# Performance work log

Measured on AMD Instinct MI355X. Metric: run time of the kernel, lower is better.

Reference implementation:

```python
import jax, jax.numpy as jnp
import numpy as np

B, S, DIM = 2, 2048, 2048
H = 16
Q_LORA, KV_LORA = 512, 512
D_NOPE, D_ROPE, D_V = 128, 64, 128
D_QK = D_NOPE + D_ROPE  # 192
SCALE = D_QK ** -0.5
EPS = 1e-6


def rmsnorm(x, w):
    return x * jax.lax.rsqrt(jnp.mean(x * x, axis=-1, keepdims=True) + EPS) * w


def apply_rope(x, cos, sin):
    # x: [B, S, h, d] with d even; cos/sin: [S, d//2] (complex-pair rotation)
    xs = x.reshape(*x.shape[:-1], -1, 2)
    x0, x1 = xs[..., 0], xs[..., 1]
    c = cos[None, :, None, :]
    s = sin[None, :, None, :]
    out = jnp.stack([x0 * c - x1 * s, x0 * s + x1 * c], axis=-1)
    return out.reshape(x.shape)


def setup_inputs() -> dict:
    key = jax.random.key(0)
    ks = jax.random.split(key, 8)
    std = 0.02
    x = jax.random.normal(ks[0], (B, S, DIM), dtype=jnp.float32)
    wq_a_w = jax.random.normal(ks[1], (DIM, Q_LORA), dtype=jnp.float32) * std
    wq_a_b = jnp.zeros((Q_LORA,), dtype=jnp.float32)
    q_norm_w = jnp.ones((Q_LORA,), dtype=jnp.float32)
    wq_b_w = jax.random.normal(ks[2], (Q_LORA, H * D_QK), dtype=jnp.float32) * std
    wkv_a_w = jax.random.normal(ks[3], (DIM, KV_LORA + D_ROPE), dtype=jnp.float32) * std
    wkv_a_b = jnp.zeros((KV_LORA + D_ROPE,), dtype=jnp.float32)
    kv_norm_w = jnp.ones((KV_LORA,), dtype=jnp.float32)
    wkv_b_w = jax.random.normal(ks[4], (KV_LORA, H * (D_NOPE + D_V)), dtype=jnp.float32) * std
    wo_w = jax.random.normal(ks[5], (H * D_V, DIM), dtype=jnp.float32) * std
    # rotary table: freqs_cis[t, i] = exp(1j * t * 10000^{-2i/d})
    inv_freq = 1.0 / (10000.0 ** (np.arange(0, D_ROPE, 2, dtype=np.float32) / D_ROPE))
    t = np.arange(S, dtype=np.float32)
    ang = np.outer(t, inv_freq)  # [S, D_ROPE//2]
    freqs_cos = jnp.asarray(np.cos(ang), dtype=jnp.float32)
    freqs_sin = jnp.asarray(np.sin(ang), dtype=jnp.float32)
    # causal mask (prefill): 0 on/below diagonal, -1e9 above
    mask = jnp.where(jnp.arange(S)[:, None] >= jnp.arange(S)[None, :], 0.0, -1e9).astype(jnp.float32)
    return {"x": x, "wq_a_w": wq_a_w, "wq_a_b": wq_a_b, "q_norm_w": q_norm_w,
            "wq_b_w": wq_b_w, "wkv_a_w": wkv_a_w, "wkv_a_b": wkv_a_b,
            "kv_norm_w": kv_norm_w, "wkv_b_w": wkv_b_w, "wo_w": wo_w,
            "freqs_cos": freqs_cos, "freqs_sin": freqs_sin, "mask": mask,
            "start_pos": 0}


def reference(x, wq_a_w, wq_a_b, q_norm_w, wq_b_w, wkv_a_w, wkv_a_b,
              kv_norm_w, wkv_b_w, wo_w, freqs_cos, freqs_sin, mask, start_pos):
    bsz, seqlen, _ = x.shape
    # low-rank Q: wq_b(q_norm(wq_a(x)))
    q = rmsnorm(x @ wq_a_w + wq_a_b, q_norm_w) @ wq_b_w
    q = q.reshape(bsz, seqlen, H, D_QK)
    q_nope, q_pe = q[..., :D_NOPE], q[..., D_NOPE:]
    q_pe = apply_rope(q_pe, freqs_cos, freqs_sin)
    # low-rank KV
    kv_full = x @ wkv_a_w + wkv_a_b
    kv, k_pe = kv_full[..., :KV_LORA], kv_full[..., KV_LORA:]
    k_pe = apply_rope(k_pe[:, :, None, :], freqs_cos, freqs_sin)  # [B,S,1,D_ROPE]
    kv = rmsnorm(kv, kv_norm_w) @ wkv_b_w
    kv = kv.reshape(bsz, seqlen, H, D_NOPE + D_V)
    k_nope, v = kv[..., :D_NOPE], kv[..., D_NOPE:]
    k = jnp.concatenate([k_nope, jnp.broadcast_to(k_pe, (bsz, seqlen, H, D_ROPE))], axis=-1)
    # prefill (start_pos=0): cache[:, :end_pos] == freshly written k, v
    q = jnp.concatenate([q_nope, q_pe], axis=-1)
    scores = jnp.einsum('bshd,bthd->bsht', q, k) * SCALE
    scores = scores + mask[None, :, None, :]
    attn = jax.nn.softmax(scores.astype(jnp.float32), axis=-1).astype(q.dtype)
    out = jnp.einsum('bsht,bthd->bshd', attn, v)
    return out.reshape(bsz, seqlen, H * D_V) @ wo_w
```

## Files before the change

kernel.cpp:

```cpp
#include <hip/hip_runtime.h>
#include <hip/hip_bf16.h>

typedef unsigned short u16;
typedef unsigned int u32;
typedef __attribute__((ext_vector_type(8))) __bf16 bf16x8;
typedef __attribute__((ext_vector_type(4))) float f32x4;
typedef __attribute__((ext_vector_type(4))) u32 u32x4;
typedef __attribute__((ext_vector_type(2))) u32 u32x2;

#define S_LEN 2048
#define BF16_ONE 0x3F80u

__device__ __forceinline__ float b2f(u16 u) {
  union { unsigned u; float f; } v; v.u = ((unsigned)u) << 16; return v.f;
}
__device__ __forceinline__ u16 f2b(float f) {
  union { float f; unsigned u; } v; v.f = f;
  unsigned r = v.u + 0x7fffu + ((v.u >> 16) & 1u);
  return (u16)(r >> 16);
}
__device__ __forceinline__ u32 cvt_pk_bf16(float a, float b) {
  u32 r;
  asm("v_cvt_pk_bf16_f32 %0, %1, %2" : "=v"(r) : "v"(a), "v"(b));
  return r;
}

__device__ __forceinline__ void glds16(const u16* g, u16* l) {
  __builtin_amdgcn_global_load_lds((const __attribute__((address_space(1))) void*)g,
                                   (__attribute__((address_space(3))) void*)l, 16, 0, 0);
}

__device__ __forceinline__ bool probe_f32(const u16* p) { return p[0] != (u16)BF16_ONE; }

struct CvtDesc {
  const void* src[7];
  u16* dst[7];
  int cum[8];
};
__global__ __launch_bounds__(256) void cvt_batch(CvtDesc d, const u16* __restrict__ probe,
                                                 int total) {
  int i = blockIdx.x * 256 + threadIdx.x;
  if (i >= total) return;
  int t = 0;
#pragma unroll
  for (int k = 1; k < 7; ++k) t += (i >= d.cum[k]);
  int li = i - d.cum[t];
  if (probe_f32(probe)) {
    const float* s = (const float*)d.src[t] + (long)li * 8;
    u16 tmp[8];
#pragma unroll
    for (int j = 0; j < 8; ++j) tmp[j] = f2b(s[j]);
    *(u32x4*)(d.dst[t] + (long)li * 8) = *(const u32x4*)tmp;
  } else {
    *(u32x4*)(d.dst[t] + (long)li * 8) = ((const u32x4*)d.src[t])[li];
  }
}

struct TrDesc {
  const void* in[5];
  u16* out[5];
  int R[5], C[5];
  int tcum[6];
  float scale[5];
};
__global__ __launch_bounds__(256) void transpose_batch(TrDesc d,
                                                       const u16* __restrict__ probe) {
  __shared__ u16 tile[32][33];
  int bid = blockIdx.x;
  int t = 0;
#pragma unroll
  for (int k = 1; k < 5; ++k) t += (bid >= d.tcum[k]);
  int rem = bid - d.tcum[t];
  const int R = d.R[t], C = d.C[t];
  const int tilesX = C >> 5;
  const int bx = rem % tilesX, by = rem / tilesX;
  const int c0 = bx * 32, r0 = by * 32;
  const int tx = threadIdx.x, ty = threadIdx.y;
  const float sc = d.scale[t];
  if (probe_f32(probe)) {
    const float* inf = (const float*)d.in[t];
#pragma unroll
    for (int i = 0; i < 4; ++i)
      tile[ty + i * 8][tx] = f2b(inf[(long)(r0 + ty + i * 8) * C + c0 + tx] * sc);
  } else {
    const u16* inb = (const u16*)d.in[t];
#pragma unroll
    for (int i = 0; i < 4; ++i)
      tile[ty + i * 8][tx] = f2b(b2f(inb[(long)(r0 + ty + i * 8) * C + c0 + tx]) * sc);
  }
  __syncthreads();
  u16* outp = d.out[t];
#pragma unroll
  for (int i = 0; i < 4; ++i)
    outp[(long)(c0 + ty + i * 8) * R + r0 + tx] = tile[tx][ty + i * 8];
}

__global__ __launch_bounds__(256) void transpose_v(const u16* __restrict__ kvb,
                                                   u16* __restrict__ vt) {
  __shared__ u16 tile[32][33];
  int s0 = blockIdx.x * 32, d0 = blockIdx.y * 32, bh = blockIdx.z;
  int b = bh >> 4, h = bh & 15;
  int tx = threadIdx.x, ty = threadIdx.y;
#pragma unroll
  for (int i = 0; i < 4; ++i)
    tile[ty + i * 8][tx] =
        kvb[((long)b * S_LEN + s0 + ty + i * 8) * 4096 + h * 256 + 128 + d0 + tx];
  __syncthreads();
#pragma unroll
  for (int i = 0; i < 4; ++i)
    vt[((long)bh * 128 + d0 + ty + i * 8) * S_LEN + s0 + tx] = tile[tx][ty + i * 8];
}

template <int MT>
__global__ __launch_bounds__(256) void gemm_bt(const u16* __restrict__ A,
                                               const u16* __restrict__ Bt,
                                               const u16* __restrict__ bias,
                                               void* __restrict__ Cv,
                                               int M, int N, int K,
                                               const u16* __restrict__ oprobe) {
  constexpr int MI = MT / 32;
  __shared__ u16 As[2][MT * 32];
  __shared__ u16 Bs[2][128 * 32];
  const int tid = threadIdx.x;
  const int lane = tid & 63;
  const int w = tid >> 6;
  const int quad = lane >> 4;
  const int l16 = lane & 15;
  const int m0 = blockIdx.y * MT;
  const int n0 = blockIdx.x * 128;
  const int wm = (w >> 1) * (MT / 2);
  const int wn = (w & 1) * 64;

  const f32x4 zero = {0.f, 0.f, 0.f, 0.f};
  f32x4 acc[MI][4];
#pragma unroll
  for (int i = 0; i < MI; ++i)
#pragma unroll
    for (int j = 0; j < 4; ++j) acc[i][j] = zero;

  auto stage = [&](int k0, int buf) {
#pragma unroll
    for (int cc = 0; cc < MT * 4; cc += 256) {
      int j = cc + tid, ar = j >> 2, ak = ((j & 3) ^ (ar & 3)) * 8;
      glds16(A + (long)(m0 + ar) * K + k0 + ak, As[buf] + j * 8);
    }
#pragma unroll
    for (int cc = 0; cc < 512; cc += 256) {
      int j = cc + tid, br = j >> 2, bk = ((j & 3) ^ (br & 3)) * 8;
      int bn = n0 + br; if (bn > N - 1) bn = N - 1;
      glds16(Bt + (long)bn * K + k0 + bk, Bs[buf] + j * 8);
    }
  };

  const int nk = K >> 5;
  stage(0, 0);
  for (int t = 0; t < nk; ++t) {
    __syncthreads();
    if (t + 1 < nk) stage((t + 1) << 5, (t + 1) & 1);
    const u16* as = As[t & 1];
    const u16* bs = Bs[t & 1];
    bf16x8 af[MI], bfr[4];
#pragma unroll
    for (int mi = 0; mi < MI; ++mi)
      af[mi] = *(const bf16x8*)(as + (wm + mi * 16 + l16) * 32 +
                                ((quad ^ (l16 & 3)) * 8));
#pragma unroll
    for (int ni = 0; ni < 4; ++ni)
      bfr[ni] = *(const bf16x8*)(bs + (wn + ni * 16 + l16) * 32 +
                                 ((quad ^ (l16 & 3)) * 8));
#pragma unroll
    for (int mi = 0; mi < MI; ++mi)
#pragma unroll
      for (int ni = 0; ni < 4; ++ni)
        acc[mi][ni] = __builtin_amdgcn_mfma_f32_16x16x32_bf16(af[mi], bfr[ni],
                                                              acc[mi][ni], 0, 0, 0);
  }

  u16* C = (u16*)Cv;
  float* Cf = (float*)Cv;
  const bool of32 = oprobe && probe_f32(oprobe);
#pragma unroll
  for (int ni = 0; ni < 4; ++ni) {
    int col = n0 + wn + ni * 16 + l16;
    if (col >= N) continue;
    float bv = bias ? b2f(bias[col]) : 0.0f;
#pragma unroll
    for (int mi = 0; mi < MI; ++mi) {
      int row = m0 + wm + mi * 16 + quad * 4;
#pragma unroll
      for (int r = 0; r < 4; ++r) {
        float val = acc[mi][ni][r] + bv;
        if (of32) Cf[(long)(row + r) * N + col] = val;
        else      C[(long)(row + r) * N + col] = f2b(val);
      }
    }
  }
}

__global__ __launch_bounds__(256) void rmsnorm512(const u16* __restrict__ in, int in_stride,
                                                  const u16* __restrict__ w,
                                                  u16* __restrict__ out, int out_stride) {
  __shared__ float red[4];
  int row = blockIdx.x, tid = threadIdx.x;
  const u16* x = in + (long)row * in_stride;
  float v0 = b2f(x[tid]), v1 = b2f(x[tid + 256]);
  float ss = v0 * v0 + v1 * v1;
#pragma unroll
  for (int off = 1; off < 64; off <<= 1) ss += __shfl_xor(ss, off);
  if ((tid & 63) == 0) red[tid >> 6] = ss;
  __syncthreads();
  float tot = red[0] + red[1] + red[2] + red[3];
  float r = rsqrtf(tot * (1.0f / 512.0f) + 1e-6f);
  u16* y = out + (long)row * out_stride;
  y[tid] = f2b(v0 * r * b2f(w[tid]));
  y[tid + 256] = f2b(v1 * r * b2f(w[tid + 256]));
}

__global__ __launch_bounds__(256) void rope_q_kernel(u16* __restrict__ q,
                                                     const u16* __restrict__ fc,
                                                     const u16* __restrict__ fs) {
  int i = blockIdx.x * 256 + threadIdx.x;
  int pair = i & 31;
  int h = (i >> 5) & 15;
  int row = i >> 9;
  int pos = row & (S_LEN - 1);
  long base = (long)row * 3072 + h * 192 + 128 + pair * 2;
  float x0 = b2f(q[base]), x1 = b2f(q[base + 1]);
  float c = b2f(fc[pos * 32 + pair]), s = b2f(fs[pos * 32 + pair]);
  q[base] = f2b(x0 * c - x1 * s);
  q[base + 1] = f2b(x0 * s + x1 * c);
}

__global__ __launch_bounds__(256) void rope_k_kernel(const u16* __restrict__ kva,
                                                     u16* __restrict__ kpe,
                                                     const u16* __restrict__ fc,
                                                     const u16* __restrict__ fs) {
  int i = blockIdx.x * 256 + threadIdx.x;
  int pair = i & 31;
  int row = i >> 5;
  int pos = row & (S_LEN - 1);
  long sb = (long)row * 576 + 512 + pair * 2;
  float x0 = b2f(kva[sb]), x1 = b2f(kva[sb + 1]);
  float c = b2f(fc[pos * 32 + pair]), s = b2f(fs[pos * 32 + pair]);
  kpe[(long)row * 64 + pair * 2] = f2b(x0 * c - x1 * s);
  kpe[(long)row * 64 + pair * 2 + 1] = f2b(x0 * s + x1 * c);
}

__global__ __launch_bounds__(512, 1) void mla_attn(const u16* __restrict__ q,
                                                   const u16* __restrict__ kvb,
                                                   const u16* __restrict__ vt,
                                                   const u16* __restrict__ kpe,
                                                   u16* __restrict__ o) {
  __shared__ u16 Ks[2][2][64 * 192];
  __shared__ u16 Vts[2][128 * 64];
  const int tid = threadIdx.x;
  const int w = tid >> 6;
  const int g = w >> 2;
  const int sw = w & 3;
  const int lane = tid & 63;
  const int quad = lane >> 4;
  const int l16 = lane & 15;
  const int bh = blockIdx.x;
  const int b = bh >> 4, h = bh & 15;
  const long rowbase = (long)b * S_LEN;
  const f32x4 zero = {0.f, 0.f, 0.f, 0.f};

  auto stage_k = [&](int t0s, u16* dst) {
#pragma unroll
    for (int tt = 0; tt < 3; ++tt) {
      int j = tt * 512 + tid;
      int r = j / 24, csw = j % 24;
      int c = csw ^ (r & 7);
      const u16* src = (c < 16)
                           ? (kvb + (rowbase + t0s + r) * 4096 + h * 256 + c * 8)
                           : (kpe + (rowbase + t0s + r) * 64 + (c - 16) * 8);
      glds16(src, dst + j * 8);
    }
  };
  auto stage_v = [&](int t0s, u16* dst) {
#pragma unroll
    for (int tt = 0; tt < 2; ++tt) {
      int j = tt * 512 + tid;
      int d = j >> 3, c = (j & 7) ^ (d & 7);
      glds16(vt + ((long)bh * 128 + d) * S_LEN + t0s + c * 8, dst + j * 8);
    }
  };

  const int srcA = (((quad & 1) << 1) | (quad >> 1)) * 16 + l16;
  const int srcB = srcA ^ 16;
  const bool lowq = quad < 2;
  const int p = quad & 1;

  const int yy = blockIdx.y;
  const int jt = (yy < 8) ? yy : 23 - yy;
  const int q0 = jt * 128;
  const int ns = jt + 1;
  const int rowlo = q0 + sw * 32;

  const u16* qrowA = q + (rowbase + rowlo + l16) * 3072 + h * 192;
  const u16* qrowB = qrowA + 16 * 3072;
  bf16x8 qfA[6], qfB[6];
#pragma unroll
  for (int kk = 0; kk < 6; ++kk) {
    qfA[kk] = *(const bf16x8*)(qrowA + kk * 32 + quad * 8);
    qfB[kk] = *(const bf16x8*)(qrowB + kk * 32 + quad * 8);
  }

  float mA = -INFINITY, mB = -INFINITY;
  float lA = 0.f, lB = 0.f;
  f32x4 oA[8], oB[8];
#pragma unroll
  for (int i = 0; i < 8; ++i) { oA[i] = zero; oB[i] = zero; }

  auto finish_half = [&](f32x4* s, float& m_r, float& l_r, f32x4* oacc,
                         int lim, bool needmask, bf16x8& ap0, bf16x8& ap1) {
    if (needmask) {
#pragma unroll
      for (int gg = 0; gg < 4; ++gg)
#pragma unroll
        for (int r = 0; r < 4; ++r)
          s[gg][r] = (gg * 16 + r > lim) ? -1e30f : s[gg][r];
    }
    float mx0 = fmaxf(fmaxf(s[0][0], s[0][1]), fmaxf(s[0][2], s[0][3]));
    float mx1 = fmaxf(fmaxf(s[1][0], s[1][1]), fmaxf(s[1][2], s[1][3]));
    float mx2 = fmaxf(fmaxf(s[2][0], s[2][1]), fmaxf(s[2][2], s[2][3]));
    float mx3 = fmaxf(fmaxf(s[3][0], s[3][1]), fmaxf(s[3][2], s[3][3]));
    float vmax = fmaxf(fmaxf(mx0, mx1), fmaxf(mx2, mx3));
    vmax = fmaxf(vmax, __shfl_xor(vmax, 16));
    vmax = fmaxf(vmax, __shfl_xor(vmax, 32));

    if (!__all(vmax <= m_r + 8.0f)) {
      float mnew = fmaxf(m_r, vmax);
      float alpha = __expf(m_r - mnew);
      m_r = mnew;
      l_r *= alpha;
      float al0 = __shfl(alpha, (lane & 48) | (quad * 4 + 0));
      float al1 = __shfl(alpha, (lane & 48) | (quad * 4 + 1));
      float al2 = __shfl(alpha, (lane & 48) | (quad * 4 + 2));
      float al3 = __shfl(alpha, (lane & 48) | (quad * 4 + 3));
#pragma unroll
      for (int nt = 0; nt < 8; ++nt) {
        f32x4 tt = oacc[nt];
        tt[0] *= al0; tt[1] *= al1; tt[2] *= al2; tt[3] *= al3;
        oacc[nt] = tt;
      }
    }

    float e00 = __expf(s[0][0] - m_r), e01 = __expf(s[0][1] - m_r);
    float e02 = __expf(s[0][2] - m_r), e03 = __expf(s[0][3] - m_r);
    float e10 = __expf(s[1][0] - m_r), e11 = __expf(s[1][1] - m_r);
    float e12 = __expf(s[1][2] - m_r), e13 = __expf(s[1][3] - m_r);
    float e20 = __expf(s[2][0] - m_r), e21 = __expf(s[2][1] - m_r);
    float e22 = __expf(s[2][2] - m_r), e23 = __expf(s[2][3] - m_r);
    float e30 = __expf(s[3][0] - m_r), e31 = __expf(s[3][1] - m_r);
    float e32 = __expf(s[3][2] - m_r), e33 = __expf(s[3][3] - m_r);
    l_r += ((e00 + e01) + (e02 + e03)) + ((e10 + e11) + (e12 + e13)) +
           ((e20 + e21) + (e22 + e23)) + ((e30 + e31) + (e32 + e33));
    u32 pk0x = cvt_pk_bf16(e00, e01), pk0y = cvt_pk_bf16(e02, e03);
    u32 pk1x = cvt_pk_bf16(e10, e11), pk1y = cvt_pk_bf16(e12, e13);
    u32 pk2x = cvt_pk_bf16(e20, e21), pk2y = cvt_pk_bf16(e22, e23);
    u32 pk3x = cvt_pk_bf16(e30, e31), pk3y = cvt_pk_bf16(e32, e33);

    u32 a0c = p ? pk1x : pk0x, a1c = p ? pk1y : pk0y;
    u32 a2c = p ? pk3x : pk2x, a3c = p ? pk3y : pk2y;
    u32 b0c = p ? pk0x : pk1x, b1c = p ? pk0y : pk1y;
    u32 b2c = p ? pk2x : pk3x, b3c = p ? pk2y : pk3y;
    u32 A0 = __shfl(a0c, srcA), A1 = __shfl(a1c, srcA);
    u32 A2 = __shfl(a2c, srcA), A3 = __shfl(a3c, srcA);
    u32 B0 = __shfl(b0c, srcB), B1 = __shfl(b1c, srcB);
    u32 B2 = __shfl(b2c, srcB), B3 = __shfl(b3c, srcB);
    u32x4 w0 = {lowq ? A0 : B0, lowq ? A1 : B1, lowq ? B0 : A0, lowq ? B1 : A1};
    u32x4 w1 = {lowq ? A2 : B2, lowq ? A3 : B3, lowq ? B2 : A2, lowq ? B3 : A3};
    ap0 = __builtin_bit_cast(bf16x8, w0);
    ap1 = __builtin_bit_cast(bf16x8, w1);
  };

  stage_k(0, Ks[0][0]);
  stage_k(64, Ks[0][1]);

  for (int i = 0; i < ns; ++i) {
    __syncthreads();
    stage_v((2 * i) * 64, Vts[0]);
    stage_v((2 * i + 1) * 64, Vts[1]);
    if (i + 1 < ns) {
      stage_k((2 * i + 2) * 64, Ks[(i + 1) & 1][0]);
      stage_k((2 * i + 3) * 64, Ks[(i + 1) & 1][1]);
    }
    const int t0 = (2 * i + g) * 64;
    const bool active = (rowlo + 31 >= t0);
    bf16x8 apA0, apA1, apB0, apB1;
    if (active) {
      const u16* ks = Ks[i & 1][g];
      f32x4 sA[4] = {zero, zero, zero, zero};
      f32x4 sB[4] = {zero, zero, zero, zero};
      __builtin_amdgcn_s_setprio(1);
#pragma unroll
      for (int kk = 0; kk < 6; ++kk) {
        const int csw = ((kk * 4 + quad) ^ (l16 & 7)) * 8;
#pragma unroll
        for (int gg = 0; gg < 4; ++gg) {
          bf16x8 kf = *(const bf16x8*)(ks + (gg * 16 + l16) * 192 + csw);
          sA[gg] = __builtin_amdgcn_mfma_f32_16x16x32_bf16(kf, qfA[kk], sA[gg], 0, 0, 0);
          sB[gg] = __builtin_amdgcn_mfma_f32_16x16x32_bf16(kf, qfB[kk], sB[gg], 0, 0, 0);
        }
      }
      __builtin_amdgcn_s_setprio(0);

      const bool nmA = (t0 + 63 > rowlo);
      const bool nmB = (t0 + 63 > rowlo + 16);
      const int limA = rowlo + l16 - t0 - quad * 4;
      finish_half(sA, mA, lA, oA, limA, nmA, apA0, apA1);
      finish_half(sB, mB, lB, oB, limA + 16, nmB, apB0, apB1);
    }
    __syncthreads();
    if (active) {
      const u16* vs = Vts[g];
      __builtin_amdgcn_s_setprio(1);
#pragma unroll
      for (int nt = 0; nt < 8; ++nt) {
        bf16x8 bv0 = *(const bf16x8*)(vs + (nt * 16 + l16) * 64 +
                                      ((quad ^ (l16 & 7)) * 8));
        bf16x8 bv1 = *(const bf16x8*)(vs + (nt * 16 + l16) * 64 +
                                      (((4 + quad) ^ (l16 & 7)) * 8));
        oA[nt] = __builtin_amdgcn_mfma_f32_16x16x32_bf16(apA0, bv0, oA[nt], 0, 0, 0);
        oA[nt] = __builtin_amdgcn_mfma_f32_16x16x32_bf16(apA1, bv1, oA[nt], 0, 0, 0);
        oB[nt] = __builtin_amdgcn_mfma_f32_16x16x32_bf16(apB0, bv0, oB[nt], 0, 0, 0);
        oB[nt] = __builtin_amdgcn_mfma_f32_16x16x32_bf16(apB1, bv1, oB[nt], 0, 0, 0);
      }
      __builtin_amdgcn_s_setprio(0);
    }
  }

  float lsA = lA; lsA += __shfl_xor(lsA, 16); lsA += __shfl_xor(lsA, 32);
  float lsB = lB; lsB += __shfl_xor(lsB, 16); lsB += __shfl_xor(lsB, 32);

  float* zone = (float*)&Ks[0][0][0];
  float* mlz = zone + 16384;
  if (g == 1) {
    float* zp0 = zone + ((sw * 2 + 0) * 64 + lane) * 32;
    float* zp1 = zone + ((sw * 2 + 1) * 64 + lane) * 32;
#pragma unroll
    for (int nt = 0; nt < 8; ++nt) {
      *(f32x4*)(zp0 + nt * 4) = oA[nt];
      *(f32x4*)(zp1 + nt * 4) = oB[nt];
    }
    mlz[((sw * 2 + 0) * 64 + lane) * 2 + 0] = mA;
    mlz[((sw * 2 + 0) * 64 + lane) * 2 + 1] = lsA;
    mlz[((sw * 2 + 1) * 64 + lane) * 2 + 0] = mB;
    mlz[((sw * 2 + 1) * 64 + lane) * 2 + 1] = lsB;
  }
  __syncthreads();
  if (g == 0) {
    auto merge_write = [&](float m_r, float ls, f32x4* oacc, int hz) {
      const float* zp = zone + ((sw * 2 + hz) * 64 + lane) * 32;
      float mo = mlz[((sw * 2 + hz) * 64 + lane) * 2 + 0];
      float lo = mlz[((sw * 2 + hz) * 64 + lane) * 2 + 1];
      float mm = fmaxf(m_r, mo);
      float aA = __expf(m_r - mm);
      float aB = __expf(mo - mm);
      float lt = ls * aA + lo * aB;
      float sAl = __fdividef(aA, lt);
      float sBl = __fdividef(aB, lt);
      float sa[4], sb[4];
#pragma unroll
      for (int r = 0; r < 4; ++r) {
        int src = (lane & 48) | (quad * 4 + r);
        sa[r] = __shfl(sAl, src);
        sb[r] = __shfl(sBl, src);
      }
      const long orow = rowbase + q0 + sw * 32 + hz * 16 + quad * 4;
#pragma unroll
      for (int nt = 0; nt < 8; ++nt) {
        f32x4 op = *(const f32x4*)(zp + nt * 4);
#pragma unroll
        for (int r = 0; r < 4; ++r)
          o[(orow + r) * 2048 + h * 128 + nt * 16 + l16] =
              f2b(oacc[nt][r] * sa[r] + op[r] * sb[r]);
      }
    };
    merge_write(mA, lsA, oA, 0);
    merge_write(mB, lsB, oB, 1);
  }
}

extern "C" void kernel_launch(void* const* d_in, const int* in_sizes, int n_in,
                              void* d_out, int out_size, void* d_ws, size_t ws_size,
                              hipStream_t stream) {
  const void* x_raw    = d_in[0];
  const void* wqa_raw  = d_in[1];
  const void* wqab_raw = d_in[2];
  const void* qnw_raw  = d_in[3];
  const void* wqb_raw  = d_in[4];
  const void* wkva_raw = d_in[5];
  const void* wkvab_raw= d_in[6];
  const void* kvnw_raw = d_in[7];
  const void* wkvb_raw = d_in[8];
  const void* wo_raw   = d_in[9];
  const void* fc_raw   = d_in[10];
  const void* fs_raw   = d_in[11];
  const u16* probe = (const u16*)qnw_raw;
  const float SC = 0.07216878364870323f;

  char* ws = (char*)d_ws;
  size_t off = 0;
  auto alloc = [&](size_t n) { void* p = ws + off; off += (n + 255) & ~(size_t)255; return p; };
  u16* xb     = (u16*)alloc(4096ull * 2048 * 2);
  u16* fcb    = (u16*)alloc(2048ull * 32 * 2);
  u16* fsb    = (u16*)alloc(2048ull * 32 * 2);
  u16* wqab_b = (u16*)alloc(512ull * 2);
  u16* qnw_b  = (u16*)alloc(512ull * 2);
  u16* wkvab_b= (u16*)alloc(576ull * 2);
  u16* kvnw_b = (u16*)alloc(512ull * 2);
  u16* wqa_t  = (u16*)alloc(512ull * 2048 * 2);
  u16* wqb_t  = (u16*)alloc(3072ull * 512 * 2);
  u16* wkva_t = (u16*)alloc(576ull * 2048 * 2);
  u16* wkvb_t = (u16*)alloc(4096ull * 512 * 2);
  u16* wo_t   = (u16*)alloc(2048ull * 2048 * 2);
  u16* qa     = (u16*)alloc(4096ull * 512 * 2);
  u16* qbuf   = (u16*)alloc(4096ull * 3072 * 2);
  u16* kva    = (u16*)alloc(4096ull * 576 * 2);
  u16* kvn    = (u16*)alloc(4096ull * 512 * 2);
  u16* kpe    = (u16*)alloc(4096ull * 64 * 2);
  u16* kvb    = (u16*)alloc(4096ull * 4096 * 2);
  u16* vtb    = (u16*)alloc(32ull * 128 * 2048 * 2);
  u16* attn   = (u16*)alloc(4096ull * 2048 * 2);

  CvtDesc cd;
  const void* csrc[7] = {x_raw, fc_raw, fs_raw, wqab_raw, qnw_raw, wkvab_raw, kvnw_raw};
  u16* cdst[7] = {xb, fcb, fsb, wqab_b, qnw_b, wkvab_b, kvnw_b};
  long cn[7] = {4096l * 2048, 2048l * 32, 2048l * 32, 512, 512, 576, 512};
  int cum = 0;
  for (int i = 0; i < 7; ++i) {
    cd.src[i] = csrc[i]; cd.dst[i] = cdst[i];
    cd.cum[i] = cum; cum += (int)(cn[i] / 8);
  }
  cd.cum[7] = cum;
  cvt_batch<<<(cum + 255) / 256, 256, 0, stream>>>(cd, probe, cum);

  TrDesc td;
  const void* tin[5] = {wqa_raw, wqb_raw, wkva_raw, wkvb_raw, wo_raw};
  u16* tout[5] = {wqa_t, wqb_t, wkva_t, wkvb_t, wo_t};
  int tR[5] = {2048, 512, 2048, 512, 2048};
  int tC[5] = {512, 3072, 576, 4096, 2048};
  float tsc[5] = {1.0f, SC, 1.0f, 1.0f, 1.0f};
  int tcum = 0;
  for (int i = 0; i < 5; ++i) {
    td.in[i] = tin[i]; td.out[i] = tout[i];
    td.R[i] = tR[i]; td.C[i] = tC[i]; td.scale[i] = tsc[i];
    td.tcum[i] = tcum; tcum += (tR[i] / 32) * (tC[i] / 32);
  }
  td.tcum[5] = tcum;
  transpose_batch<<<tcum, dim3(32, 8), 0, stream>>>(td, probe);

  gemm_bt<64><<<dim3(4, 64), 256, 0, stream>>>(xb, wqa_t, wqab_b, qa, 4096, 512, 2048, nullptr);
  rmsnorm512<<<4096, 256, 0, stream>>>(qa, 512, qnw_b, qa, 512);
  gemm_bt<128><<<dim3(24, 32), 256, 0, stream>>>(qa, wqb_t, nullptr, qbuf, 4096, 3072, 512, nullptr);
  rope_q_kernel<<<8192, 256, 0, stream>>>(qbuf, fcb, fsb);

  gemm_bt<64><<<dim3(5, 64), 256, 0, stream>>>(xb, wkva_t, wkvab_b, kva, 4096, 576, 2048, nullptr);
  rmsnorm512<<<4096, 256, 0, stream>>>(kva, 576, kvnw_b, kvn, 512);
  rope_k_kernel<<<512, 256, 0, stream>>>(kva, kpe, fcb, fsb);
  gemm_bt<128><<<dim3(32, 32), 256, 0, stream>>>(kvn, wkvb_t, nullptr, kvb, 4096, 4096, 512, nullptr);
  transpose_v<<<dim3(64, 4, 32), dim3(32, 8), 0, stream>>>(kvb, vtb);

  mla_attn<<<dim3(32, 16), 512, 0, stream>>>(qbuf, kvb, vtb, kpe, attn);

  gemm_bt<128><<<dim3(16, 32), 256, 0, stream>>>(attn, wo_t, nullptr, d_out, 4096, 2048, 2048, probe);
}
```

Measured before the change: 426.5 us.

## Fuse the Q and KV down-projection GEMMs and swizzle the LDS merge buffer

The wq_a and wkv_a weights are transposed into one concatenated 1088-wide matrix with a combined bias. A single GEMM over x then produces both latent projections, where before two separate GEMMs each read x. The rmsnorm and rope_k kernels now read from offsets inside the fused output. The split-K merge zone in the attention epilogue also gets an XOR swizzle on its f32x4 slots to cut LDS bank conflicts. One risk: 1088 is not a multiple of the 128-wide tile, so correctness depends on the GEMM handling a partial N tile.

```diff
diff --git a/kernel.cpp b/kernel.cpp
--- a/kernel.cpp
+++ b/kernel.cpp
@@ -231,7 +231,7 @@
   q[base + 1] = f2b(x0 * s + x1 * c);
 }
 
-__global__ __launch_bounds__(256) void rope_k_kernel(const u16* __restrict__ kva,
+__global__ __launch_bounds__(256) void rope_k_kernel(const u16* __restrict__ qkva,
                                                      u16* __restrict__ kpe,
                                                      const u16* __restrict__ fc,
                                                      const u16* __restrict__ fs) {
@@ -239,8 +239,8 @@
   int pair = i & 31;
   int row = i >> 5;
   int pos = row & (S_LEN - 1);
-  long sb = (long)row * 576 + 512 + pair * 2;
-  float x0 = b2f(kva[sb]), x1 = b2f(kva[sb + 1]);
+  long sb = (long)row * 1088 + 1024 + pair * 2;
+  float x0 = b2f(qkva[sb]), x1 = b2f(qkva[sb + 1]);
   float c = b2f(fc[pos * 32 + pair]), s = b2f(fs[pos * 32 + pair]);
   kpe[(long)row * 64 + pair * 2] = f2b(x0 * c - x1 * s);
   kpe[(long)row * 64 + pair * 2 + 1] = f2b(x0 * s + x1 * c);
@@ -441,8 +441,8 @@
     float* zp1 = zone + ((sw * 2 + 1) * 64 + lane) * 32;
 #pragma unroll
     for (int nt = 0; nt < 8; ++nt) {
-      *(f32x4*)(zp0 + nt * 4) = oA[nt];
-      *(f32x4*)(zp1 + nt * 4) = oB[nt];
+      *(f32x4*)(zp0 + ((nt ^ (lane & 7)) << 2)) = oA[nt];
+      *(f32x4*)(zp1 + ((nt ^ (lane & 7)) << 2)) = oB[nt];
     }
     mlz[((sw * 2 + 0) * 64 + lane) * 2 + 0] = mA;
     mlz[((sw * 2 + 0) * 64 + lane) * 2 + 1] = lsA;
@@ -471,7 +471,7 @@
       const long orow = rowbase + q0 + sw * 32 + hz * 16 + quad * 4;
 #pragma unroll
       for (int nt = 0; nt < 8; ++nt) {
-        f32x4 op = *(const f32x4*)(zp + nt * 4);
+        f32x4 op = *(const f32x4*)(zp + ((nt ^ (lane & 7)) << 2));
 #pragma unroll
         for (int r = 0; r < 4; ++r)
           o[(orow + r) * 2048 + h * 128 + nt * 16 + l16] =
@@ -507,18 +507,16 @@
   u16* xb     = (u16*)alloc(4096ull * 2048 * 2);
   u16* fcb    = (u16*)alloc(2048ull * 32 * 2);
   u16* fsb    = (u16*)alloc(2048ull * 32 * 2);
-  u16* wqab_b = (u16*)alloc(512ull * 2);
+  u16* biasc  = (u16*)alloc(1088ull * 2);
   u16* qnw_b  = (u16*)alloc(512ull * 2);
-  u16* wkvab_b= (u16*)alloc(576ull * 2);
   u16* kvnw_b = (u16*)alloc(512ull * 2);
-  u16* wqa_t  = (u16*)alloc(512ull * 2048 * 2);
+  u16* qkvat  = (u16*)alloc(1088ull * 2048 * 2);
   u16* wqb_t  = (u16*)alloc(3072ull * 512 * 2);
-  u16* wkva_t = (u16*)alloc(576ull * 2048 * 2);
   u16* wkvb_t = (u16*)alloc(4096ull * 512 * 2);
   u16* wo_t   = (u16*)alloc(2048ull * 2048 * 2);
+  u16* qkva   = (u16*)alloc(4096ull * 1088 * 2);
   u16* qa     = (u16*)alloc(4096ull * 512 * 2);
   u16* qbuf   = (u16*)alloc(4096ull * 3072 * 2);
-  u16* kva    = (u16*)alloc(4096ull * 576 * 2);
   u16* kvn    = (u16*)alloc(4096ull * 512 * 2);
   u16* kpe    = (u16*)alloc(4096ull * 64 * 2);
   u16* kvb    = (u16*)alloc(4096ull * 4096 * 2);
@@ -527,7 +525,7 @@
 
   CvtDesc cd;
   const void* csrc[7] = {x_raw, fc_raw, fs_raw, wqab_raw, qnw_raw, wkvab_raw, kvnw_raw};
-  u16* cdst[7] = {xb, fcb, fsb, wqab_b, qnw_b, wkvab_b, kvnw_b};
+  u16* cdst[7] = {xb, fcb, fsb, biasc, qnw_b, biasc + 512, kvnw_b};
   long cn[7] = {4096l * 2048, 2048l * 32, 2048l * 32, 512, 512, 576, 512};
   int cum = 0;
   for (int i = 0; i < 7; ++i) {
@@ -539,7 +537,7 @@
 
   TrDesc td;
   const void* tin[5] = {wqa_raw, wqb_raw, wkva_raw, wkvb_raw, wo_raw};
-  u16* tout[5] = {wqa_t, wqb_t, wkva_t, wkvb_t, wo_t};
+  u16* tout[5] = {qkvat, wqb_t, qkvat + 512ull * 2048, wkvb_t, wo_t};
   int tR[5] = {2048, 512, 2048, 512, 2048};
   int tC[5] = {512, 3072, 576, 4096, 2048};
   float tsc[5] = {1.0f, SC, 1.0f, 1.0f, 1.0f};
@@ -552,14 +550,14 @@
   td.tcum[5] = tcum;
   transpose_batch<<<tcum, dim3(32, 8), 0, stream>>>(td, probe);
 
-  gemm_bt<64><<<dim3(4, 64), 256, 0, stream>>>(xb, wqa_t, wqab_b, qa, 4096, 512, 2048, nullptr);
-  rmsnorm512<<<4096, 256, 0, stream>>>(qa, 512, qnw_b, qa, 512);
+  gemm_bt<128><<<dim3(9, 32), 256, 0, stream>>>(xb, qkvat, biasc, qkva, 4096, 1088, 2048, nullptr);
+
+  rmsnorm512<<<4096, 256, 0, stream>>>(qkva, 1088, qnw_b, qa, 512);
   gemm_bt<128><<<dim3(24, 32), 256, 0, stream>>>(qa, wqb_t, nullptr, qbuf, 4096, 3072, 512, nullptr);
   rope_q_kernel<<<8192, 256, 0, stream>>>(qbuf, fcb, fsb);
 
-  gemm_bt<64><<<dim3(5, 64), 256, 0, stream>>>(xb, wkva_t, wkvab_b, kva, 4096, 576, 2048, nullptr);
-  rmsnorm512<<<4096, 256, 0, stream>>>(kva, 576, kvnw_b, kvn, 512);
-  rope_k_kernel<<<512, 256, 0, stream>>>(kva, kpe, fcb, fsb);
+  rmsnorm512<<<4096, 256, 0, stream>>>(qkva + 512, 1088, kvnw_b, kvn, 512);
+  rope_k_kernel<<<512, 256, 0, stream>>>(qkva, kpe, fcb, fsb);
   gemm_bt<128><<<dim3(32, 32), 256, 0, stream>>>(kvn, wkvb_t, nullptr, kvb, 4096, 4096, 512, nullptr);
   transpose_v<<<dim3(64, 4, 32), dim3(32, 8), 0, stream>>>(kvb, vtb);
 
```

Measured after the change: 403.0 us. -5.5%, faster.
